# Kernel optimization log

Measured on AMD Instinct MI355X. Metric: run time of the kernel, lower is better.

Reference implementation:

```python
import jax, jax.numpy as jnp
import numpy as np

IN_CH, OUT_CH, SUPPORT = 128, 128, 3
BS, N = 8, 2048


def knn_idx(x, k):
    # x: (bs, n, d) -> (bs, n, k) indices of k nearest (excluding self)
    sq = jnp.sum(x * x, axis=-1)  # (bs, n)
    dist = sq[:, :, None] + sq[:, None, :] - 2.0 * jnp.einsum('bnd,bmd->bnm', x, x)
    _, idx = jax.lax.top_k(-dist, k + 1)  # smallest distances
    return idx[:, :, 1:]


def gather_neighbors(t, idx):
    # t: (bs, n, d), idx: (bs, n, k) -> (bs, n, k, d)
    return jax.vmap(lambda tb, ib: tb[ib])(t, idx)


def l2_normalize(x, axis, eps=1e-12):
    n = jnp.linalg.norm(x, axis=axis, keepdims=True)
    return x / jnp.maximum(n, eps)


def setup_inputs() -> dict:
    key = jax.random.key(0)
    ks = jax.random.split(key, 8)
    stdv = 1.0 / np.sqrt(OUT_CH * (SUPPORT + 1))
    return {
        'vertices': jax.random.normal(ks[0], (BS, N, 3), jnp.float32),
        'feature_map': jax.random.normal(ks[1], (BS, N, IN_CH), jnp.float32),
        'weights': jax.random.uniform(ks[2], (IN_CH, (SUPPORT + 1) * OUT_CH), jnp.float32, -stdv, stdv),
        'bias': jax.random.uniform(ks[3], ((SUPPORT + 1) * OUT_CH,), jnp.float32, -stdv, stdv),
        'directions': jax.random.uniform(ks[4], (3, SUPPORT * OUT_CH), jnp.float32, -stdv, stdv),
        'ste_w': jax.random.normal(ks[5], (OUT_CH, IN_CH), jnp.float32) * (1.0 / np.sqrt(IN_CH)),
        'conv2_w': jax.random.normal(ks[6], (OUT_CH, 2 * OUT_CH), jnp.float32) * (1.0 / np.sqrt(2 * OUT_CH)),
        'neighbor_num': 16,
    }


def reference(vertices, feature_map, weights, bias, directions, ste_w, conv2_w, neighbor_num):
    bs, n, _ = vertices.shape
    k = neighbor_num

    # STE branch: 1x1 conv == per-point linear
    f_ste = jnp.einsum('bnc,oc->bno', feature_map, ste_w)

    # Receptive fields: KNN in feature space ('RF-F'), directions from vertices
    neighbor_index = knn_idx(feature_map, k)                      # (bs, n, k)
    neighbors = gather_neighbors(vertices, neighbor_index)        # (bs, n, k, 3)
    rf_norm = l2_normalize(neighbors - vertices[:, :, None, :], axis=-1)

    # Graph convolution (3D-GCN style)
    sdn = l2_normalize(directions, axis=0)                        # (3, s*out)
    theta = jax.nn.relu(jnp.einsum('bnkd,dm->bnkm', rf_norm, sdn))  # (bs,n,k,s*out)
    fm = feature_map @ weights + bias                             # (bs,n,(s+1)*out)
    feature_center = fm[:, :, :OUT_CH]
    feature_support = gather_neighbors(fm[:, :, OUT_CH:], neighbor_index)  # (bs,n,k,s*out)
    act = (theta * feature_support).reshape(bs, n, k, SUPPORT, OUT_CH)
    act = jnp.max(act, axis=2)          # max over neighbors
    act = jnp.mean(act, axis=2)         # mean over supports
    feature = feature_center + act      # (bs, n, out)

    # ORL: global context via point-space KNN max-pool
    nb_idx2 = knn_idx(vertices, k)
    pooled = jnp.max(gather_neighbors(feature, nb_idx2), axis=2)  # (bs,n,out)
    f_global = jnp.broadcast_to(jnp.mean(pooled, axis=1, keepdims=True), (bs, n, OUT_CH))
    feat_cat = jnp.concatenate([feature, f_global], axis=-1)      # (bs,n,2*out)
    feature_fuse = jnp.einsum('bnc,oc->bno', feat_cat, conv2_w) + feature

    return feature_fuse + f_ste
```

## Files before the change

### kernel.cpp

```cpp
#include <hip/hip_runtime.h>
#include <hip/hip_bf16.h>

#define BS 8
#define NP 2048
#define CIN 128
#define OC 128
#define NSUP 3
#define KNN 16
#define NC 512
#define SC 384
#define CAND 24

typedef __attribute__((ext_vector_type(8))) short bf16x8;
typedef __attribute__((ext_vector_type(4))) float f32x4;

__device__ inline unsigned short f2bf(float x) {
    __hip_bfloat16 h = __float2bfloat16(x);
    return *reinterpret_cast<unsigned short*>(&h);
}
__device__ inline float bf2f(short s) {
    unsigned u = ((unsigned)(unsigned short)s) << 16;
    return __uint_as_float(u);
}
__device__ inline unsigned fkey(float d, int gi) {
    unsigned u = __float_as_uint(d);
    u ^= (unsigned)((int)u >> 31) | 0x80000000u;
    return (u & 0xFFFFF800u) | (unsigned)gi;
}
__device__ inline unsigned umn(unsigned a, unsigned b) { return a < b ? a : b; }
__device__ inline unsigned umx(unsigned a, unsigned b) { return a > b ? a : b; }
__device__ inline void cswap(unsigned& a, unsigned& b) {
    unsigned t = umn(a, b); b = umx(a, b); a = t;
}
__device__ inline unsigned dpp_prev(unsigned v) {
    return (unsigned)__builtin_amdgcn_update_dpp(0, (int)v, 0x111, 0xF, 0xF, true);
}
__device__ inline unsigned third_smallest8(const unsigned kv[8]) {
    unsigned s0=kv[0],s1=kv[1],s2=kv[2],s3=kv[3],s4=kv[4],s5=kv[5],s6=kv[6],s7=kv[7];
    cswap(s0,s1); cswap(s2,s3); cswap(s4,s5); cswap(s6,s7);
    cswap(s0,s2); cswap(s1,s3); cswap(s4,s6); cswap(s5,s7);
    cswap(s1,s2); cswap(s5,s6); cswap(s0,s4); cswap(s3,s7);
    cswap(s1,s5); cswap(s2,s6);
    cswap(s1,s4); cswap(s3,s6);
    cswap(s2,s4); cswap(s3,s5);
    cswap(s3,s4);
    return s2;
}

__global__ __launch_bounds__(256) void prep_kernel(const float* __restrict__ in,
                                                   float* __restrict__ sq,
                                                   short* __restrict__ outp,
                                                   const float* __restrict__ W,
                                                   const float* __restrict__ conv2,
                                                   const float* __restrict__ stew,
                                                   const float* __restrict__ dirs,
                                                   short* __restrict__ Wt,
                                                   short* __restrict__ conv2b,
                                                   short* __restrict__ stewb,
                                                   float4* __restrict__ sdnn4) {
    const int tid = threadIdx.x;
    if (blockIdx.x < 1024) {
        const int row = blockIdx.x * 16 + (tid >> 4);
        const int seg = tid & 15;
        const float* p = in + (size_t)row * CIN + seg * 8;
        float4 f0 = *(const float4*)p;
        float4 f1 = *(const float4*)(p + 4);
        bf16x8 s;
        s[0] = (short)f2bf(f0.x); s[1] = (short)f2bf(f0.y);
        s[2] = (short)f2bf(f0.z); s[3] = (short)f2bf(f0.w);
        s[4] = (short)f2bf(f1.x); s[5] = (short)f2bf(f1.y);
        s[6] = (short)f2bf(f1.z); s[7] = (short)f2bf(f1.w);
        *(bf16x8*)&outp[(size_t)row * CIN + seg * 8] = s;
        float ss = f0.x*f0.x + f0.y*f0.y + f0.z*f0.z + f0.w*f0.w
                 + f1.x*f1.x + f1.y*f1.y + f1.z*f1.z + f1.w*f1.w;
#pragma unroll
        for (int msk = 1; msk <= 8; msk <<= 1) ss += __shfl_xor(ss, msk);
        if (seg == 0) sq[row] = ss;
    } else if (blockIdx.x < 1472) {
        int idx = (blockIdx.x - 1024) * 256 + tid;
        if (idx < NC * CIN) {
            int n = idx >> 7, k = idx & 127;
            Wt[idx] = (short)f2bf(W[(size_t)k * NC + n]);
        } else if (idx < NC * CIN + OC * 2 * OC) {
            int e = idx - NC * CIN;
            conv2b[e] = (short)f2bf(conv2[e]);
        } else {
            int e = idx - NC * CIN - OC * 2 * OC;
            stewb[e] = (short)f2bf(stew[e]);
        }
    } else {
        int m = (blockIdx.x - 1472) * 256 + tid;
        if (m < SC) {
            float d0 = dirs[m], d1 = dirs[SC + m], d2 = dirs[2 * SC + m];
            float nrm = sqrtf(d0 * d0 + d1 * d1 + d2 * d2);
            float den = fmaxf(nrm, 1e-12f);
            sdnn4[m] = make_float4(d0 / den, d1 / den, d2 / den, 0.f);
        }
    }
}

#define TQF 32
#define TPF 64
#define NCHF (NP / TPF)
#define SMEM_BYTES 33536
__global__ __launch_bounds__(256) void fused_kernel(const short* __restrict__ fbb,
                                                    const float* __restrict__ sqn,
                                                    int* __restrict__ cand,
                                                    const float* __restrict__ vert,
                                                    int* __restrict__ nbr2,
                                                    const short* __restrict__ Wt,
                                                    const float* __restrict__ bias,
                                                    float* __restrict__ centerf,
                                                    short* __restrict__ supb) {
    __shared__ alignas(16) unsigned char smem[SMEM_BYTES];
    const int bx = blockIdx.x;
    const int tid = threadIdx.x;
    const int lane = tid & 63, wid = tid >> 6;

    if (bx < 512) {
        short (*Qb)[128]   = (short (*)[128])smem;
        short (*Pb)[128]   = (short (*)[128])(smem + 8192);
        float* sqP         = (float*)(smem + 24576);
        unsigned (*Ds)[68] = (unsigned (*)[68])(smem + 24832);

        const int b = bx >> 6, q0 = (bx & 63) * TQF;
        const short* fb = fbb + (size_t)b * NP * CIN;

        unsigned l0 = 0xFFFFFFFFu, l1 = 0xFFFFFFFFu, l2 = 0xFFFFFFFFu;
        unsigned T = 0xFFFFFFFFu;
        const int gbase = lane & 56;
        const int sub = lane & 7;

        for (int i = 0; i < 2; ++i) {
            int v = i * 256 + tid, row = v >> 4, g = v & 15;
            *(bf16x8*)&Qb[row][(g ^ (row & 7)) * 8] =
                *(const bf16x8*)&fb[(size_t)(q0 + row) * CIN + g * 8];
        }
        for (int i = 0; i < 4; ++i) {
            int v = i * 256 + tid, row = v >> 4, g = v & 15;
            *(bf16x8*)&Pb[row][(g ^ (row & 7)) * 8] =
                *(const bf16x8*)&fb[(size_t)row * CIN + g * 8];
        }
        if (tid < TPF) sqP[tid] = sqn[b * NP + tid];

        const int qt = wid >> 1, ph = wid & 1;
        const int qsl = tid >> 3;
        const int arow = qt * 16 + (lane & 15), asw = arow & 7;
        const int brow0 = ph * 32 + (lane & 15), brow1 = brow0 + 16;
        const int bsw0 = brow0 & 7, bsw1 = brow1 & 7;
        const int oct = lane >> 4;
        const int qrow = qt * 16 + oct * 4;

        for (int ch = 0; ch < NCHF; ++ch) {
            __syncthreads();
            bf16x8 st0, st1, st2, st3;
            float sq_next = 0.f;
            const int nxt = (ch + 1 < NCHF);
            if (nxt) {
                int p0n = (ch + 1) * TPF;
                { int v = tid;       int row = v>>4, g = v&15; st0 = *(const bf16x8*)&fb[(size_t)(p0n+row)*CIN + g*8]; }
                { int v = 256 + tid; int row = v>>4, g = v&15; st1 = *(const bf16x8*)&fb[(size_t)(p0n+row)*CIN + g*8]; }
                { int v = 512 + tid; int row = v>>4, g = v&15; st2 = *(const bf16x8*)&fb[(size_t)(p0n+row)*CIN + g*8]; }
                { int v = 768 + tid; int row = v>>4, g = v&15; st3 = *(const bf16x8*)&fb[(size_t)(p0n+row)*CIN + g*8]; }
                if (tid < TPF) sq_next = sqn[b * NP + p0n + tid];
            }
            f32x4 acc0 = {0.f,0.f,0.f,0.f}, acc1 = {0.f,0.f,0.f,0.f};
#pragma unroll
            for (int kk = 0; kk < 4; ++kk) {
                int g = kk * 4 + oct;
                bf16x8 av  = *(const bf16x8*)&Qb[arow][(g ^ asw) * 8];
                bf16x8 bv0 = *(const bf16x8*)&Pb[brow0][(g ^ bsw0) * 8];
                bf16x8 bv1 = *(const bf16x8*)&Pb[brow1][(g ^ bsw1) * 8];
                acc0 = __builtin_amdgcn_mfma_f32_16x16x32_bf16(av, bv0, acc0, 0, 0, 0);
                acc1 = __builtin_amdgcn_mfma_f32_16x16x32_bf16(av, bv1, acc1, 0, 0, 0);
            }
            const float sp0 = sqP[brow0], sp1 = sqP[brow1];
            const int pg0 = ch * TPF + brow0, pg1 = ch * TPF + brow1;
#pragma unroll
            for (int r = 0; r < 4; ++r) {
                int qg = q0 + qrow + r;
                unsigned k0 = fkey(sp0 - 2.0f * acc0[r], pg0);
                unsigned k1 = fkey(sp1 - 2.0f * acc1[r], pg1);
                if (qg == pg0) k0 = 0xFFFFFFFFu;
                if (qg == pg1) k1 = 0xFFFFFFFFu;
                Ds[qrow + r][brow0] = k0;
                Ds[qrow + r][brow1] = k1;
            }
            __syncthreads();
            {
                uint4 kA = *(const uint4*)&Ds[qsl][sub * 8];
                uint4 kB = *(const uint4*)&Ds[qsl][sub * 8 + 4];
                unsigned kv[8] = {kA.x, kA.y, kA.z, kA.w, kB.x, kB.y, kB.z, kB.w};
                if (ch == 0) {
                    unsigned m3 = third_smallest8(kv);
                    m3 = umx(m3, (unsigned)__shfl_xor((int)m3, 1));
                    m3 = umx(m3, (unsigned)__shfl_xor((int)m3, 2));
                    m3 = umx(m3, (unsigned)__shfl_xor((int)m3, 4));
                    T = m3 + 1;
                }
#pragma unroll
                for (int j = 0; j < 8; ++j) {
                    unsigned long long bal = __ballot(kv[j] < T);
                    unsigned gm = (unsigned)(bal >> gbase) & 0xFFu;
                    while (gm) {
                        int l = __builtin_ctz(gm);
                        gm &= gm - 1;
                        unsigned k = (unsigned)__shfl((int)kv[j], gbase + l);
                        unsigned pv = dpp_prev(l2);
                        if (sub == 0) pv = 0u;
                        unsigned n0 = umn(umx(pv, k), l0);
                        unsigned n1 = umn(umx(l0, k), l1);
                        unsigned n2 = umn(umx(l1, k), l2);
                        l0 = n0; l1 = n1; l2 = n2;
                    }
                }
                T = (unsigned)__shfl((int)l2, gbase + 7);
            }
            if (nxt) {
                { int v = tid;       int row = v>>4, g = v&15; *(bf16x8*)&Pb[row][(g^(row&7))*8] = st0; }
                { int v = 256 + tid; int row = v>>4, g = v&15; *(bf16x8*)&Pb[row][(g^(row&7))*8] = st1; }
                { int v = 512 + tid; int row = v>>4, g = v&15; *(bf16x8*)&Pb[row][(g^(row&7))*8] = st2; }
                { int v = 768 + tid; int row = v>>4, g = v&15; *(bf16x8*)&Pb[row][(g^(row&7))*8] = st3; }
                if (tid < TPF) sqP[tid] = sq_next;
            }
        }
        {
            int* dst = cand + ((size_t)b * NP + q0 + qsl) * CAND;
            dst[3 * sub + 0] = (int)(l0 & 0x7FFu);
            dst[3 * sub + 1] = (int)(l1 & 0x7FFu);
            dst[3 * sub + 2] = (int)(l2 & 0x7FFu);
        }
    } else if (bx < 1024) {
        float* vx = (float*)smem;
        float* vy = (float*)(smem + 8192);
        float* vz = (float*)(smem + 16384);
        const int bb = bx - 512;
        const int b = bb >> 6, q0 = (bb & 63) * 32;
        const float* vb = vert + (size_t)b * NP * 3;

        for (int i = 0; i < NP * 3 / 256; ++i) {
            int e = i * 256 + tid;
            float v = vb[e];
            int row = e / 3, comp = e % 3;
            (comp == 0 ? vx : comp == 1 ? vy : vz)[row] = v;
        }
        __syncthreads();

        const int gbase = lane & 56;
        const int q = tid >> 3;
        const int sub = tid & 7;
        const float qx = vx[q0 + q], qy = vy[q0 + q], qz = vz[q0 + q];

        unsigned l0 = 0xFFFFFFFFu, l1 = 0xFFFFFFFFu, l2 = 0xFFFFFFFFu;
        unsigned T = 0xFFFFFFFFu;

        for (int m = 0; m < NP / 64; ++m) {
            const int p0 = m * 64 + sub * 8;
            float4 xA = *(const float4*)&vx[p0], xB = *(const float4*)&vx[p0 + 4];
            float4 yA = *(const float4*)&vy[p0], yB = *(const float4*)&vy[p0 + 4];
            float4 zA = *(const float4*)&vz[p0], zB = *(const float4*)&vz[p0 + 4];
            float dv[8];
            { float dx = qx-xA.x, dy = qy-yA.x, dz = qz-zA.x; dv[0] = dx*dx+dy*dy+dz*dz; }
            { float dx = qx-xA.y, dy = qy-yA.y, dz = qz-zA.y; dv[1] = dx*dx+dy*dy+dz*dz; }
            { float dx = qx-xA.z, dy = qy-yA.z, dz = qz-zA.z; dv[2] = dx*dx+dy*dy+dz*dz; }
            { float dx = qx-xA.w, dy = qy-yA.w, dz = qz-zA.w; dv[3] = dx*dx+dy*dy+dz*dz; }
            { float dx = qx-xB.x, dy = qy-yB.x, dz = qz-zB.x; dv[4] = dx*dx+dy*dy+dz*dz; }
            { float dx = qx-xB.y, dy = qy-yB.y, dz = qz-zB.y; dv[5] = dx*dx+dy*dy+dz*dz; }
            { float dx = qx-xB.z, dy = qy-yB.z, dz = qz-zB.z; dv[6] = dx*dx+dy*dy+dz*dz; }
            { float dx = qx-xB.w, dy = qy-yB.w, dz = qz-zB.w; dv[7] = dx*dx+dy*dy+dz*dz; }
            unsigned kv[8];
#pragma unroll
            for (int j = 0; j < 8; ++j) kv[j] = fkey(dv[j], p0 + j);
            if (m == 0) {
                unsigned m3 = third_smallest8(kv);
                m3 = umx(m3, (unsigned)__shfl_xor((int)m3, 1));
                m3 = umx(m3, (unsigned)__shfl_xor((int)m3, 2));
                m3 = umx(m3, (unsigned)__shfl_xor((int)m3, 4));
                T = m3 + 1;
            }
#pragma unroll
            for (int j = 0; j < 8; ++j) {
                unsigned long long bal = __ballot(kv[j] < T);
                unsigned gm = (unsigned)(bal >> gbase) & 0xFFu;
                while (gm) {
                    int l = __builtin_ctz(gm);
                    gm &= gm - 1;
                    unsigned k = (unsigned)__shfl((int)kv[j], gbase + l);
                    unsigned pv = dpp_prev(l2);
                    if (sub == 0) pv = 0u;
                    unsigned n0 = umn(umx(pv, k), l0);
                    unsigned n1 = umn(umx(l0, k), l1);
                    unsigned n2 = umn(umx(l1, k), l2);
                    l0 = n0; l1 = n1; l2 = n2;
                }
            }
            T = (unsigned)__shfl((int)l2, gbase + 7);
        }
        {
            int* dst = nbr2 + ((size_t)b * NP + q0 + q) * KNN;
            unsigned vals[3] = {l0, l1, l2};
#pragma unroll
            for (int e = 0; e < 3; ++e) {
                int r = 3 * sub + e;
                if (r >= 1 && r <= 16) dst[r - 1] = (int)(vals[e] & 0x7FFu);
            }
        }
    } else {
        short (*As)[128] = (short (*)[128])smem;
        const int bb = bx - 1024;
        const int m0 = (bb & 255) * 64, n0 = (bb >> 8) * 128;
        const int oct = lane >> 4;
        for (int i = 0; i < 4; ++i) {
            int v = i * 256 + tid, row = v >> 4, g = v & 15;
            *(bf16x8*)&As[row][(g ^ (row & 7)) * 8] =
                *(const bf16x8*)&fbb[(size_t)(m0 + row) * CIN + g * 8];
        }
        __syncthreads();
        f32x4 acc[4][2] = {};
#pragma unroll
        for (int kk = 0; kk < 4; ++kk) {
            int g = kk * 4 + oct;
            bf16x8 bv[2];
#pragma unroll
            for (int nt = 0; nt < 2; ++nt) {
                int n = n0 + (wid * 2 + nt) * 16 + (lane & 15);
                bv[nt] = *(const bf16x8*)&Wt[(size_t)n * CIN + g * 8];
            }
#pragma unroll
            for (int mt = 0; mt < 4; ++mt) {
                int ar = mt * 16 + (lane & 15);
                bf16x8 av = *(const bf16x8*)&As[ar][(g ^ (ar & 7)) * 8];
#pragma unroll
                for (int nt = 0; nt < 2; ++nt)
                    acc[mt][nt] = __builtin_amdgcn_mfma_f32_16x16x32_bf16(av, bv[nt], acc[mt][nt], 0, 0, 0);
            }
        }
#pragma unroll
        for (int mt = 0; mt < 4; ++mt)
#pragma unroll
            for (int nt = 0; nt < 2; ++nt) {
                int n = n0 + (wid * 2 + nt) * 16 + (lane & 15);
                float bsv = bias[n];
                int mbase = m0 + mt * 16 + oct * 4;
#pragma unroll
                for (int r = 0; r < 4; ++r) {
                    float val = acc[mt][nt][r] + bsv;
                    if (n0 == 0)
                        centerf[(size_t)(mbase + r) * OC + n] = val;
                    else
                        supb[(size_t)(mbase + r) * SC + (n - OC)] = (short)f2bf(val);
                }
            }
    }
}

__global__ __launch_bounds__(256) void knn_refine_kernel(const float* __restrict__ feat,
                                                         const int* __restrict__ cand,
                                                         int* __restrict__ nbr) {
    __shared__ unsigned long long keyS[4][CAND];
    const int w = threadIdx.x >> 6;
    const int lane = threadIdx.x & 63;
    const int grp = lane >> 4, sl = lane & 15;
    const int gq = blockIdx.x * 4 + w;
    const int b = gq >> 11;
    const int q = gq & (NP - 1);
    const float* fb = feat + (size_t)b * NP * CIN;

    double qd[8];
    {
        float4 a = *(const float4*)&fb[(size_t)q * CIN + sl * 8];
        float4 c = *(const float4*)&fb[(size_t)q * CIN + sl * 8 + 4];
        qd[0] = a.x; qd[1] = a.y; qd[2] = a.z; qd[3] = a.w;
        qd[4] = c.x; qd[5] = c.y; qd[6] = c.z; qd[7] = c.w;
    }
    double sqd = 0.0;
#pragma unroll
    for (int i = 0; i < 8; ++i) sqd += qd[i] * qd[i];
#pragma unroll
    for (int msk = 1; msk <= 8; msk <<= 1) sqd += __shfl_xor(sqd, msk);
    const float sqi = (float)sqd;

    const int* cq = cand + (size_t)gq * CAND;
    int jv[CAND / 4];
#pragma unroll
    for (int t = 0; t < CAND / 4; ++t) jv[t] = cq[t * 4 + grp];

#pragma unroll
    for (int t = 0; t < CAND / 4; ++t) {
        const int j = jv[t];
        float4 a = *(const float4*)&fb[(size_t)j * CIN + sl * 8];
        float4 c = *(const float4*)&fb[(size_t)j * CIN + sl * 8 + 4];
        double fd[8] = {a.x, a.y, a.z, a.w, c.x, c.y, c.z, c.w};
        double dot = 0.0, sj = 0.0;
#pragma unroll
        for (int i = 0; i < 8; ++i) { dot += qd[i] * fd[i]; sj += fd[i] * fd[i]; }
#pragma unroll
        for (int msk = 1; msk <= 8; msk <<= 1) {
            dot += __shfl_xor(dot, msk);
            sj  += __shfl_xor(sj, msk);
        }
        if (sl == 0) {
            float t1 = sqi + (float)sj;
            float t2 = (float)(2.0 * dot);
            float d32 = t1 - t2;
            unsigned u = __float_as_uint(d32);
            u ^= (unsigned)((int)u >> 31) | 0x80000000u;
            keyS[w][t * 4 + grp] = ((unsigned long long)u << 32) | (unsigned)j;
        }
    }
    __syncthreads();
    if (lane < CAND) {
        unsigned long long k = keyS[w][lane];
        int rank = 0;
#pragma unroll
        for (int m = 0; m < CAND; ++m) rank += (keyS[w][m] < k) ? 1 : 0;
        if (rank < KNN) nbr[(size_t)gq * KNN + rank] = (int)(k & 0xFFFFFFFFu);
    }
}

__global__ __launch_bounds__(128) void act_kernel(const float* __restrict__ centerf,
                                                  const short* __restrict__ supb,
                                                  const int* __restrict__ nbr,
                                                  const float* __restrict__ vert,
                                                  const float4* __restrict__ sdnn4,
                                                  float* __restrict__ feature,
                                                  short* __restrict__ featb) {
    __shared__ int sj[KNN];
    __shared__ float rf[KNN][4];
    const int i = blockIdx.x;
    const int b = blockIdx.y;
    const int tid = threadIdx.x;
    const size_t bi = (size_t)b * NP + i;
    if (tid < KNN) {
        int j = nbr[bi * KNN + tid];
        sj[tid] = j;
        const float* vb = vert + (size_t)b * NP * 3;
        float dx = vb[j * 3 + 0] - vb[i * 3 + 0];
        float dy = vb[j * 3 + 1] - vb[i * 3 + 1];
        float dz = vb[j * 3 + 2] - vb[i * 3 + 2];
        float nrm = sqrtf(dx * dx + dy * dy + dz * dz);
        float den = fmaxf(nrm, 1e-12f);
        rf[tid][0] = dx / den; rf[tid][1] = dy / den; rf[tid][2] = dz / den;
    }
    __syncthreads();
    const int oc = tid;
    float accm = 0.0f;
#pragma unroll
    for (int s = 0; s < NSUP; ++s) {
        int m = s * OC + oc;
        float4 sv = sdnn4[m];
        float s0 = sv.x, s1 = sv.y, s2 = sv.z;
        float vm[4] = {-3.0e38f, -3.0e38f, -3.0e38f, -3.0e38f};
#pragma unroll
        for (int kk = 0; kk < KNN; ++kk) {
            float th = fmaxf(rf[kk][0] * s0 + rf[kk][1] * s1 + rf[kk][2] * s2, 0.0f);
            float sup = bf2f(supb[((size_t)b * NP + sj[kk]) * SC + m]);
            vm[kk & 3] = fmaxf(vm[kk & 3], th * sup);
        }
        accm += fmaxf(fmaxf(vm[0], vm[1]), fmaxf(vm[2], vm[3]));
    }
    float v = centerf[bi * OC + oc] + accm / 3.0f;
    feature[bi * OC + oc] = v;
    featb[bi * OC + oc] = (short)f2bf(v);
}

__global__ __launch_bounds__(128) void pool_kernel(const short* __restrict__ featb,
                                                   const int* __restrict__ nbr2,
                                                   float* __restrict__ pooled) {
    __shared__ int sj[KNN];
    const int i = blockIdx.x, b = blockIdx.y, tid = threadIdx.x;
    const size_t bi = (size_t)b * NP + i;
    if (tid < KNN) sj[tid] = nbr2[bi * KNN + tid];
    __syncthreads();
    float m0 = -3.0e38f, m1 = -3.0e38f, m2 = -3.0e38f, m3 = -3.0e38f;
#pragma unroll
    for (int kk = 0; kk < KNN; kk += 4) {
        m0 = fmaxf(m0, bf2f(featb[((size_t)b * NP + sj[kk + 0]) * OC + tid]));
        m1 = fmaxf(m1, bf2f(featb[((size_t)b * NP + sj[kk + 1]) * OC + tid]));
        m2 = fmaxf(m2, bf2f(featb[((size_t)b * NP + sj[kk + 2]) * OC + tid]));
        m3 = fmaxf(m3, bf2f(featb[((size_t)b * NP + sj[kk + 3]) * OC + tid]));
    }
    pooled[bi * OC + tid] = fmaxf(fmaxf(m0, m1), fmaxf(m2, m3));
}

__global__ __launch_bounds__(128) void partial_kernel(const float* __restrict__ pooled,
                                                      float* __restrict__ part) {
    const int ch = blockIdx.x, b = blockIdx.y, tid = threadIdx.x;
    float s0 = 0.f, s1 = 0.f, s2 = 0.f, s3 = 0.f;
    const float* base = pooled + ((size_t)b * NP + ch * 128) * OC + tid;
    for (int i = 0; i < 128; i += 4) {
        s0 += base[(size_t)(i + 0) * OC];
        s1 += base[(size_t)(i + 1) * OC];
        s2 += base[(size_t)(i + 2) * OC];
        s3 += base[(size_t)(i + 3) * OC];
    }
    part[((size_t)b * 16 + ch) * OC + tid] = ((s0 + s1) + (s2 + s3));
}
__global__ __launch_bounds__(128) void fg_gdot_kernel(const float* __restrict__ part,
                                                      const float* __restrict__ conv2,
                                                      float* __restrict__ gd) {
    __shared__ float fgs[OC];
    const int b = blockIdx.x, tid = threadIdx.x;
    float s = 0.f;
#pragma unroll
    for (int c = 0; c < 16; ++c) s += part[((size_t)b * 16 + c) * OC + tid];
    fgs[tid] = s / (float)NP;
    __syncthreads();
    float g = 0.f;
    const float* w = conv2 + (size_t)tid * 2 * OC + OC;
    for (int c = 0; c < OC; ++c) g += fgs[c] * w[c];
    gd[b * OC + tid] = g;
}

__global__ __launch_bounds__(256) void final_kernel(const short* __restrict__ featb,
                                                    const short* __restrict__ fbb,
                                                    const short* __restrict__ conv2b,
                                                    const short* __restrict__ stewb,
                                                    const float* __restrict__ gd,
                                                    const float* __restrict__ feature,
                                                    float* __restrict__ out) {
    __shared__ alignas(16) short Af[32][128];
    __shared__ alignas(16) short Am[32][128];
    const int m0 = blockIdx.x * 32, tid = threadIdx.x;
    const int lane = tid & 63, wid = tid >> 6, oct = lane >> 4;
    for (int i = 0; i < 2; ++i) {
        int v = i * 256 + tid, row = v >> 4, g = v & 15;
        *(bf16x8*)&Af[row][(g ^ (row & 7)) * 8] =
            *(const bf16x8*)&featb[(size_t)(m0 + row) * OC + g * 8];
        *(bf16x8*)&Am[row][(g ^ (row & 7)) * 8] =
            *(const bf16x8*)&fbb[(size_t)(m0 + row) * CIN + g * 8];
    }
    __syncthreads();
    f32x4 acc[2][2] = {};
#pragma unroll
    for (int kk = 0; kk < 4; ++kk) {
        int g = kk * 4 + oct;
        bf16x8 bC[2], bS[2];
#pragma unroll
        for (int nt = 0; nt < 2; ++nt) {
            int n = (wid * 2 + nt) * 16 + (lane & 15);
            bC[nt] = *(const bf16x8*)&conv2b[(size_t)n * (2 * OC) + g * 8];
            bS[nt] = *(const bf16x8*)&stewb[(size_t)n * CIN + g * 8];
        }
#pragma unroll
        for (int mt = 0; mt < 2; ++mt) {
            int ar = mt * 16 + (lane & 15);
            bf16x8 aF = *(const bf16x8*)&Af[ar][(g ^ (ar & 7)) * 8];
            bf16x8 aM = *(const bf16x8*)&Am[ar][(g ^ (ar & 7)) * 8];
#pragma unroll
            for (int nt = 0; nt < 2; ++nt) {
                acc[mt][nt] = __builtin_amdgcn_mfma_f32_16x16x32_bf16(aF, bC[nt], acc[mt][nt], 0, 0, 0);
                acc[mt][nt] = __builtin_amdgcn_mfma_f32_16x16x32_bf16(aM, bS[nt], acc[mt][nt], 0, 0, 0);
            }
        }
    }
#pragma unroll
    for (int mt = 0; mt < 2; ++mt)
#pragma unroll
        for (int nt = 0; nt < 2; ++nt) {
            int o = (wid * 2 + nt) * 16 + (lane & 15);
            int mbase = m0 + mt * 16 + oct * 4;
#pragma unroll
            for (int r = 0; r < 4; ++r) {
                int m = mbase + r;
                out[(size_t)m * OC + o] = acc[mt][nt][r]
                    + gd[(m >> 11) * OC + o] + feature[(size_t)m * OC + o];
            }
        }
}

extern "C" void kernel_launch(void* const* d_in, const int* in_sizes, int n_in,
                              void* d_out, int out_size, void* d_ws, size_t ws_size,
                              hipStream_t stream) {
    const float* vert  = (const float*)d_in[0];
    const float* fmap  = (const float*)d_in[1];
    const float* W     = (const float*)d_in[2];
    const float* bias  = (const float*)d_in[3];
    const float* dirs  = (const float*)d_in[4];
    const float* stew  = (const float*)d_in[5];
    const float* conv2 = (const float*)d_in[6];
    float* out = (float*)d_out;

    float* ws      = (float*)d_ws;
    float* sqn     = ws;
    short* fbb     = (short*)(sqn + 16384);
    float* centerf = sqn + 16384 + 1048576;
    short* supb    = (short*)(centerf + 2097152);
    float* feature = centerf + 2097152 + 3145728;
    short* featb   = (short*)(feature + 2097152);
    float* gd      = feature + 2097152 + 1048576;
    short* Wt      = (short*)(gd + 1024);
    short* conv2b  = Wt + 65536;
    short* stewb   = conv2b + 32768;
    int*   nbr1    = (int*)(stewb + 16384);
    int*   nbr2    = nbr1 + 262144;
    float* part    = (float*)(nbr2 + 262144);
    float4* sdnn4  = (float4*)(part + 16384);
    int*   cand    = (int*)(sdnn4 + 384);
    float* pooled  = (float*)(cand + 393216);

    prep_kernel<<<1474, 256, 0, stream>>>(fmap, sqn, fbb, W, conv2, stew, dirs,
                                          Wt, conv2b, stewb, sdnn4);
    fused_kernel<<<2048, 256, 0, stream>>>(fbb, sqn, cand, vert, nbr2,
                                           Wt, bias, centerf, supb);
    knn_refine_kernel<<<4096, 256, 0, stream>>>(fmap, cand, nbr1);
    act_kernel<<<dim3(2048, 8), 128, 0, stream>>>(centerf, supb, nbr1, vert, sdnn4,
                                                  feature, featb);
    pool_kernel<<<dim3(2048, 8), 128, 0, stream>>>(featb, nbr2, pooled);
    partial_kernel<<<dim3(16, 8), 128, 0, stream>>>(pooled, part);
    fg_gdot_kernel<<<8, 128, 0, stream>>>(part, conv2, gd);
    final_kernel<<<512, 256, 0, stream>>>(featb, fbb, conv2b, stewb, gd, feature, out);
}
```

Before: 205.9 us.

## Split feature KNN into its own kernel and fuse refinement with vertex KNN and GEMM

The feature-space KNN candidate search moves out of the multi-role fused kernel into a dedicated 512-block kernel. The fp64 candidate refinement is merged into a second multi-role kernel alongside the vertex KNN and the weight GEMM. The aim is to let the long-running feature KNN blocks run alone, then overlap the refinement with the independent vertex KNN and GEMM work, while keeping the same number of launches. In exchange, the vertex KNN and GEMM no longer overlap with the feature KNN search, and the new kernel's shared-memory footprint changes its occupancy.

```diff
diff --git a/kernel.cpp b/kernel.cpp
--- a/kernel.cpp
+++ b/kernel.cpp
@@ -102,139 +102,204 @@
 #define TQF 32
 #define TPF 64
 #define NCHF (NP / TPF)
-#define SMEM_BYTES 33536
-__global__ __launch_bounds__(256) void fused_kernel(const short* __restrict__ fbb,
-                                                    const float* __restrict__ sqn,
-                                                    int* __restrict__ cand,
-                                                    const float* __restrict__ vert,
-                                                    int* __restrict__ nbr2,
-                                                    const short* __restrict__ Wt,
-                                                    const float* __restrict__ bias,
-                                                    float* __restrict__ centerf,
-                                                    short* __restrict__ supb) {
-    __shared__ alignas(16) unsigned char smem[SMEM_BYTES];
+__global__ __launch_bounds__(256) void knn_feat_kernel(const short* __restrict__ fbb,
+                                                       const float* __restrict__ sqn,
+                                                       int* __restrict__ cand) {
+    __shared__ alignas(16) short Qb[TQF][128];
+    __shared__ alignas(16) short Pb[TPF][128];
+    __shared__ float sqP[TPF];
+    __shared__ unsigned Ds[TQF][68];
+
+    const int b = blockIdx.y, q0 = blockIdx.x * TQF, tid = threadIdx.x;
+    const int lane = tid & 63, wid = tid >> 6;
+    const short* fb = fbb + (size_t)b * NP * CIN;
+
+    unsigned l0 = 0xFFFFFFFFu, l1 = 0xFFFFFFFFu, l2 = 0xFFFFFFFFu;
+    unsigned T = 0xFFFFFFFFu;
+    const int gbase = lane & 56;
+    const int sub = lane & 7;
+
+    for (int i = 0; i < 2; ++i) {
+        int v = i * 256 + tid, row = v >> 4, g = v & 15;
+        *(bf16x8*)&Qb[row][(g ^ (row & 7)) * 8] =
+            *(const bf16x8*)&fb[(size_t)(q0 + row) * CIN + g * 8];
+    }
+    for (int i = 0; i < 4; ++i) {
+        int v = i * 256 + tid, row = v >> 4, g = v & 15;
+        *(bf16x8*)&Pb[row][(g ^ (row & 7)) * 8] =
+            *(const bf16x8*)&fb[(size_t)row * CIN + g * 8];
+    }
+    if (tid < TPF) sqP[tid] = sqn[b * NP + tid];
+
+    const int qt = wid >> 1, ph = wid & 1;
+    const int qsl = tid >> 3;
+    const int arow = qt * 16 + (lane & 15), asw = arow & 7;
+    const int brow0 = ph * 32 + (lane & 15), brow1 = brow0 + 16;
+    const int bsw0 = brow0 & 7, bsw1 = brow1 & 7;
+    const int oct = lane >> 4;
+    const int qrow = qt * 16 + oct * 4;
+
+    for (int ch = 0; ch < NCHF; ++ch) {
+        __syncthreads();
+        bf16x8 st0, st1, st2, st3;
+        float sq_next = 0.f;
+        const int nxt = (ch + 1 < NCHF);
+        if (nxt) {
+            int p0n = (ch + 1) * TPF;
+            { int v = tid;       int row = v>>4, g = v&15; st0 = *(const bf16x8*)&fb[(size_t)(p0n+row)*CIN + g*8]; }
+            { int v = 256 + tid; int row = v>>4, g = v&15; st1 = *(const bf16x8*)&fb[(size_t)(p0n+row)*CIN + g*8]; }
+            { int v = 512 + tid; int row = v>>4, g = v&15; st2 = *(const bf16x8*)&fb[(size_t)(p0n+row)*CIN + g*8]; }
+            { int v = 768 + tid; int row = v>>4, g = v&15; st3 = *(const bf16x8*)&fb[(size_t)(p0n+row)*CIN + g*8]; }
+            if (tid < TPF) sq_next = sqn[b * NP + p0n + tid];
+        }
+        f32x4 acc0 = {0.f,0.f,0.f,0.f}, acc1 = {0.f,0.f,0.f,0.f};
+#pragma unroll
+        for (int kk = 0; kk < 4; ++kk) {
+            int g = kk * 4 + oct;
+            bf16x8 av  = *(const bf16x8*)&Qb[arow][(g ^ asw) * 8];
+            bf16x8 bv0 = *(const bf16x8*)&Pb[brow0][(g ^ bsw0) * 8];
+            bf16x8 bv1 = *(const bf16x8*)&Pb[brow1][(g ^ bsw1) * 8];
+            acc0 = __builtin_amdgcn_mfma_f32_16x16x32_bf16(av, bv0, acc0, 0, 0, 0);
+            acc1 = __builtin_amdgcn_mfma_f32_16x16x32_bf16(av, bv1, acc1, 0, 0, 0);
+        }
+        const float sp0 = sqP[brow0], sp1 = sqP[brow1];
+        const int pg0 = ch * TPF + brow0, pg1 = ch * TPF + brow1;
+#pragma unroll
+        for (int r = 0; r < 4; ++r) {
+            int qg = q0 + qrow + r;
+            unsigned k0 = fkey(sp0 - 2.0f * acc0[r], pg0);
+            unsigned k1 = fkey(sp1 - 2.0f * acc1[r], pg1);
+            if (qg == pg0) k0 = 0xFFFFFFFFu;
+            if (qg == pg1) k1 = 0xFFFFFFFFu;
+            Ds[qrow + r][brow0] = k0;
+            Ds[qrow + r][brow1] = k1;
+        }
+        __syncthreads();
+        {
+            uint4 kA = *(const uint4*)&Ds[qsl][sub * 8];
+            uint4 kB = *(const uint4*)&Ds[qsl][sub * 8 + 4];
+            unsigned kv[8] = {kA.x, kA.y, kA.z, kA.w, kB.x, kB.y, kB.z, kB.w};
+            if (ch == 0) {
+                unsigned m3 = third_smallest8(kv);
+                m3 = umx(m3, (unsigned)__shfl_xor((int)m3, 1));
+                m3 = umx(m3, (unsigned)__shfl_xor((int)m3, 2));
+                m3 = umx(m3, (unsigned)__shfl_xor((int)m3, 4));
+                T = m3 + 1;
+            }
+#pragma unroll
+            for (int j = 0; j < 8; ++j) {
+                unsigned long long bal = __ballot(kv[j] < T);
+                unsigned gm = (unsigned)(bal >> gbase) & 0xFFu;
+                while (gm) {
+                    int l = __builtin_ctz(gm);
+                    gm &= gm - 1;
+                    unsigned k = (unsigned)__shfl((int)kv[j], gbase + l);
+                    unsigned pv = dpp_prev(l2);
+                    if (sub == 0) pv = 0u;
+                    unsigned n0 = umn(umx(pv, k), l0);
+                    unsigned n1 = umn(umx(l0, k), l1);
+                    unsigned n2 = umn(umx(l1, k), l2);
+                    l0 = n0; l1 = n1; l2 = n2;
+                }
+            }
+            T = (unsigned)__shfl((int)l2, gbase + 7);
+        }
+        if (nxt) {
+            { int v = tid;       int row = v>>4, g = v&15; *(bf16x8*)&Pb[row][(g^(row&7))*8] = st0; }
+            { int v = 256 + tid; int row = v>>4, g = v&15; *(bf16x8*)&Pb[row][(g^(row&7))*8] = st1; }
+            { int v = 512 + tid; int row = v>>4, g = v&15; *(bf16x8*)&Pb[row][(g^(row&7))*8] = st2; }
+            { int v = 768 + tid; int row = v>>4, g = v&15; *(bf16x8*)&Pb[row][(g^(row&7))*8] = st3; }
+            if (tid < TPF) sqP[tid] = sq_next;
+        }
+    }
+    {
+        int* dst = cand + ((size_t)b * NP + q0 + qsl) * CAND;
+        dst[3 * sub + 0] = (int)(l0 & 0x7FFu);
+        dst[3 * sub + 1] = (int)(l1 & 0x7FFu);
+        dst[3 * sub + 2] = (int)(l2 & 0x7FFu);
+    }
+}
+
+#define SMEM2 24576
+__global__ __launch_bounds__(256) void fused2_kernel(const float* __restrict__ feat,
+                                                     const int* __restrict__ cand,
+                                                     int* __restrict__ nbr,
+                                                     const float* __restrict__ vert,
+                                                     int* __restrict__ nbr2,
+                                                     const short* __restrict__ fbb,
+                                                     const short* __restrict__ Wt,
+                                                     const float* __restrict__ bias,
+                                                     float* __restrict__ centerf,
+                                                     short* __restrict__ supb) {
+    __shared__ alignas(16) unsigned char smem[SMEM2];
     const int bx = blockIdx.x;
     const int tid = threadIdx.x;
     const int lane = tid & 63, wid = tid >> 6;
 
-    if (bx < 512) {
-        short (*Qb)[128]   = (short (*)[128])smem;
-        short (*Pb)[128]   = (short (*)[128])(smem + 8192);
-        float* sqP         = (float*)(smem + 24576);
-        unsigned (*Ds)[68] = (unsigned (*)[68])(smem + 24832);
-
-        const int b = bx >> 6, q0 = (bx & 63) * TQF;
-        const short* fb = fbb + (size_t)b * NP * CIN;
-
-        unsigned l0 = 0xFFFFFFFFu, l1 = 0xFFFFFFFFu, l2 = 0xFFFFFFFFu;
-        unsigned T = 0xFFFFFFFFu;
-        const int gbase = lane & 56;
-        const int sub = lane & 7;
-
-        for (int i = 0; i < 2; ++i) {
-            int v = i * 256 + tid, row = v >> 4, g = v & 15;
-            *(bf16x8*)&Qb[row][(g ^ (row & 7)) * 8] =
-                *(const bf16x8*)&fb[(size_t)(q0 + row) * CIN + g * 8];
-        }
-        for (int i = 0; i < 4; ++i) {
-            int v = i * 256 + tid, row = v >> 4, g = v & 15;
-            *(bf16x8*)&Pb[row][(g ^ (row & 7)) * 8] =
-                *(const bf16x8*)&fb[(size_t)row * CIN + g * 8];
-        }
-        if (tid < TPF) sqP[tid] = sqn[b * NP + tid];
-
-        const int qt = wid >> 1, ph = wid & 1;
-        const int qsl = tid >> 3;
-        const int arow = qt * 16 + (lane & 15), asw = arow & 7;
-        const int brow0 = ph * 32 + (lane & 15), brow1 = brow0 + 16;
-        const int bsw0 = brow0 & 7, bsw1 = brow1 & 7;
-        const int oct = lane >> 4;
-        const int qrow = qt * 16 + oct * 4;
-
-        for (int ch = 0; ch < NCHF; ++ch) {
-            __syncthreads();
-            bf16x8 st0, st1, st2, st3;
-            float sq_next = 0.f;
-            const int nxt = (ch + 1 < NCHF);
-            if (nxt) {
-                int p0n = (ch + 1) * TPF;
-                { int v = tid;       int row = v>>4, g = v&15; st0 = *(const bf16x8*)&fb[(size_t)(p0n+row)*CIN + g*8]; }
-                { int v = 256 + tid; int row = v>>4, g = v&15; st1 = *(const bf16x8*)&fb[(size_t)(p0n+row)*CIN + g*8]; }
-                { int v = 512 + tid; int row = v>>4, g = v&15; st2 = *(const bf16x8*)&fb[(size_t)(p0n+row)*CIN + g*8]; }
-                { int v = 768 + tid; int row = v>>4, g = v&15; st3 = *(const bf16x8*)&fb[(size_t)(p0n+row)*CIN + g*8]; }
-                if (tid < TPF) sq_next = sqn[b * NP + p0n + tid];
-            }
-            f32x4 acc0 = {0.f,0.f,0.f,0.f}, acc1 = {0.f,0.f,0.f,0.f};
-#pragma unroll
-            for (int kk = 0; kk < 4; ++kk) {
-                int g = kk * 4 + oct;
-                bf16x8 av  = *(const bf16x8*)&Qb[arow][(g ^ asw) * 8];
-                bf16x8 bv0 = *(const bf16x8*)&Pb[brow0][(g ^ bsw0) * 8];
-                bf16x8 bv1 = *(const bf16x8*)&Pb[brow1][(g ^ bsw1) * 8];
-                acc0 = __builtin_amdgcn_mfma_f32_16x16x32_bf16(av, bv0, acc0, 0, 0, 0);
-                acc1 = __builtin_amdgcn_mfma_f32_16x16x32_bf16(av, bv1, acc1, 0, 0, 0);
-            }
-            const float sp0 = sqP[brow0], sp1 = sqP[brow1];
-            const int pg0 = ch * TPF + brow0, pg1 = ch * TPF + brow1;
-#pragma unroll
-            for (int r = 0; r < 4; ++r) {
-                int qg = q0 + qrow + r;
-                unsigned k0 = fkey(sp0 - 2.0f * acc0[r], pg0);
-                unsigned k1 = fkey(sp1 - 2.0f * acc1[r], pg1);
-                if (qg == pg0) k0 = 0xFFFFFFFFu;
-                if (qg == pg1) k1 = 0xFFFFFFFFu;
-                Ds[qrow + r][brow0] = k0;
-                Ds[qrow + r][brow1] = k1;
-            }
-            __syncthreads();
-            {
-                uint4 kA = *(const uint4*)&Ds[qsl][sub * 8];
-                uint4 kB = *(const uint4*)&Ds[qsl][sub * 8 + 4];
-                unsigned kv[8] = {kA.x, kA.y, kA.z, kA.w, kB.x, kB.y, kB.z, kB.w};
-                if (ch == 0) {
-                    unsigned m3 = third_smallest8(kv);
-                    m3 = umx(m3, (unsigned)__shfl_xor((int)m3, 1));
-                    m3 = umx(m3, (unsigned)__shfl_xor((int)m3, 2));
-                    m3 = umx(m3, (unsigned)__shfl_xor((int)m3, 4));
-                    T = m3 + 1;
-                }
-#pragma unroll
-                for (int j = 0; j < 8; ++j) {
-                    unsigned long long bal = __ballot(kv[j] < T);
-                    unsigned gm = (unsigned)(bal >> gbase) & 0xFFu;
-                    while (gm) {
-                        int l = __builtin_ctz(gm);
-                        gm &= gm - 1;
-                        unsigned k = (unsigned)__shfl((int)kv[j], gbase + l);
-                        unsigned pv = dpp_prev(l2);
-                        if (sub == 0) pv = 0u;
-                        unsigned n0 = umn(umx(pv, k), l0);
-                        unsigned n1 = umn(umx(l0, k), l1);
-                        unsigned n2 = umn(umx(l1, k), l2);
-                        l0 = n0; l1 = n1; l2 = n2;
-                    }
-                }
-                T = (unsigned)__shfl((int)l2, gbase + 7);
-            }
-            if (nxt) {
-                { int v = tid;       int row = v>>4, g = v&15; *(bf16x8*)&Pb[row][(g^(row&7))*8] = st0; }
-                { int v = 256 + tid; int row = v>>4, g = v&15; *(bf16x8*)&Pb[row][(g^(row&7))*8] = st1; }
-                { int v = 512 + tid; int row = v>>4, g = v&15; *(bf16x8*)&Pb[row][(g^(row&7))*8] = st2; }
-                { int v = 768 + tid; int row = v>>4, g = v&15; *(bf16x8*)&Pb[row][(g^(row&7))*8] = st3; }
-                if (tid < TPF) sqP[tid] = sq_next;
-            }
-        }
+    if (bx < 4096) {
+        unsigned long long (*keyS)[CAND] = (unsigned long long (*)[CAND])smem;
+        const int w = wid;
+        const int grp = lane >> 4, sl = lane & 15;
+        const int gq = bx * 4 + w;
+        const int b = gq >> 11;
+        const int q = gq & (NP - 1);
+        const float* fb = feat + (size_t)b * NP * CIN;
+
+        double qd[8];
         {
-            int* dst = cand + ((size_t)b * NP + q0 + qsl) * CAND;
-            dst[3 * sub + 0] = (int)(l0 & 0x7FFu);
-            dst[3 * sub + 1] = (int)(l1 & 0x7FFu);
-            dst[3 * sub + 2] = (int)(l2 & 0x7FFu);
-        }
-    } else if (bx < 1024) {
+            float4 a = *(const float4*)&fb[(size_t)q * CIN + sl * 8];
+            float4 c = *(const float4*)&fb[(size_t)q * CIN + sl * 8 + 4];
+            qd[0] = a.x; qd[1] = a.y; qd[2] = a.z; qd[3] = a.w;
+            qd[4] = c.x; qd[5] = c.y; qd[6] = c.z; qd[7] = c.w;
+        }
+        double sqd = 0.0;
+#pragma unroll
+        for (int i = 0; i < 8; ++i) sqd += qd[i] * qd[i];
+#pragma unroll
+        for (int msk = 1; msk <= 8; msk <<= 1) sqd += __shfl_xor(sqd, msk);
+        const float sqi = (float)sqd;
+
+        const int* cq = cand + (size_t)gq * CAND;
+        int jv[CAND / 4];
+#pragma unroll
+        for (int t = 0; t < CAND / 4; ++t) jv[t] = cq[t * 4 + grp];
+
+#pragma unroll
+        for (int t = 0; t < CAND / 4; ++t) {
+            const int j = jv[t];
+            float4 a = *(const float4*)&fb[(size_t)j * CIN + sl * 8];
+            float4 c = *(const float4*)&fb[(size_t)j * CIN + sl * 8 + 4];
+            double fd[8] = {a.x, a.y, a.z, a.w, c.x, c.y, c.z, c.w};
+            double dot = 0.0, sj = 0.0;
+#pragma unroll
+            for (int i = 0; i < 8; ++i) { dot += qd[i] * fd[i]; sj += fd[i] * fd[i]; }
+#pragma unroll
+            for (int msk = 1; msk <= 8; msk <<= 1) {
+                dot += __shfl_xor(dot, msk);
+                sj  += __shfl_xor(sj, msk);
+            }
+            if (sl == 0) {
+                float t1 = sqi + (float)sj;
+                float t2 = (float)(2.0 * dot);
+                float d32 = t1 - t2;
+                unsigned u = __float_as_uint(d32);
+                u ^= (unsigned)((int)u >> 31) | 0x80000000u;
+                keyS[w][t * 4 + grp] = ((unsigned long long)u << 32) | (unsigned)j;
+            }
+        }
+        __syncthreads();
+        if (lane < CAND) {
+            unsigned long long k = keyS[w][lane];
+            int rank = 0;
+#pragma unroll
+            for (int m = 0; m < CAND; ++m) rank += (keyS[w][m] < k) ? 1 : 0;
+            if (rank < KNN) nbr[(size_t)gq * KNN + rank] = (int)(k & 0xFFFFFFFFu);
+        }
+    } else if (bx < 4608) {
         float* vx = (float*)smem;
         float* vy = (float*)(smem + 8192);
         float* vz = (float*)(smem + 16384);
-        const int bb = bx - 512;
+        const int bb = bx - 4096;
         const int b = bb >> 6, q0 = (bb & 63) * 32;
         const float* vb = vert + (size_t)b * NP * 3;
 
@@ -307,7 +372,7 @@
         }
     } else {
         short (*As)[128] = (short (*)[128])smem;
-        const int bb = bx - 1024;
+        const int bb = bx - 4608;
         const int m0 = (bb & 255) * 64, n0 = (bb >> 8) * 128;
         const int oct = lane >> 4;
         for (int i = 0; i < 4; ++i) {
@@ -351,70 +416,6 @@
                         supb[(size_t)(mbase + r) * SC + (n - OC)] = (short)f2bf(val);
                 }
             }
-    }
-}
-
-__global__ __launch_bounds__(256) void knn_refine_kernel(const float* __restrict__ feat,
-                                                         const int* __restrict__ cand,
-                                                         int* __restrict__ nbr) {
-    __shared__ unsigned long long keyS[4][CAND];
-    const int w = threadIdx.x >> 6;
-    const int lane = threadIdx.x & 63;
-    const int grp = lane >> 4, sl = lane & 15;
-    const int gq = blockIdx.x * 4 + w;
-    const int b = gq >> 11;
-    const int q = gq & (NP - 1);
-    const float* fb = feat + (size_t)b * NP * CIN;
-
-    double qd[8];
-    {
-        float4 a = *(const float4*)&fb[(size_t)q * CIN + sl * 8];
-        float4 c = *(const float4*)&fb[(size_t)q * CIN + sl * 8 + 4];
-        qd[0] = a.x; qd[1] = a.y; qd[2] = a.z; qd[3] = a.w;
-        qd[4] = c.x; qd[5] = c.y; qd[6] = c.z; qd[7] = c.w;
-    }
-    double sqd = 0.0;
-#pragma unroll
-    for (int i = 0; i < 8; ++i) sqd += qd[i] * qd[i];
-#pragma unroll
-    for (int msk = 1; msk <= 8; msk <<= 1) sqd += __shfl_xor(sqd, msk);
-    const float sqi = (float)sqd;
-
-    const int* cq = cand + (size_t)gq * CAND;
-    int jv[CAND / 4];
-#pragma unroll
-    for (int t = 0; t < CAND / 4; ++t) jv[t] = cq[t * 4 + grp];
-
-#pragma unroll
-    for (int t = 0; t < CAND / 4; ++t) {
-        const int j = jv[t];
-        float4 a = *(const float4*)&fb[(size_t)j * CIN + sl * 8];
-        float4 c = *(const float4*)&fb[(size_t)j * CIN + sl * 8 + 4];
-        double fd[8] = {a.x, a.y, a.z, a.w, c.x, c.y, c.z, c.w};
-        double dot = 0.0, sj = 0.0;
-#pragma unroll
-        for (int i = 0; i < 8; ++i) { dot += qd[i] * fd[i]; sj += fd[i] * fd[i]; }
-#pragma unroll
-        for (int msk = 1; msk <= 8; msk <<= 1) {
-            dot += __shfl_xor(dot, msk);
-            sj  += __shfl_xor(sj, msk);
-        }
-        if (sl == 0) {
-            float t1 = sqi + (float)sj;
-            float t2 = (float)(2.0 * dot);
-            float d32 = t1 - t2;
-            unsigned u = __float_as_uint(d32);
-            u ^= (unsigned)((int)u >> 31) | 0x80000000u;
-            keyS[w][t * 4 + grp] = ((unsigned long long)u << 32) | (unsigned)j;
-        }
-    }
-    __syncthreads();
-    if (lane < CAND) {
-        unsigned long long k = keyS[w][lane];
-        int rank = 0;
-#pragma unroll
-        for (int m = 0; m < CAND; ++m) rank += (keyS[w][m] < k) ? 1 : 0;
-        if (rank < KNN) nbr[(size_t)gq * KNN + rank] = (int)(k & 0xFFFFFFFFu);
     }
 }
 
@@ -601,9 +602,9 @@
 
     prep_kernel<<<1474, 256, 0, stream>>>(fmap, sqn, fbb, W, conv2, stew, dirs,
                                           Wt, conv2b, stewb, sdnn4);
-    fused_kernel<<<2048, 256, 0, stream>>>(fbb, sqn, cand, vert, nbr2,
-                                           Wt, bias, centerf, supb);
-    knn_refine_kernel<<<4096, 256, 0, stream>>>(fmap, cand, nbr1);
+    knn_feat_kernel<<<dim3(64, 8), 256, 0, stream>>>(fbb, sqn, cand);
+    fused2_kernel<<<5632, 256, 0, stream>>>(fmap, cand, nbr1, vert, nbr2,
+                                            fbb, Wt, bias, centerf, supb);
     act_kernel<<<dim3(2048, 8), 128, 0, stream>>>(centerf, supb, nbr1, vert, sdnn4,
                                                   feature, featb);
     pool_kernel<<<dim3(2048, 8), 128, 0, stream>>>(featb, nbr2, pooled);
```

Result: slower. 210.6 us (+2.3%).

## Regroup fused kernels: move point-space KNN alongside feature-KNN refine

Applied to the files above, without the earlier changes.

The point-space KNN blocks move out of the first fused kernel, which now holds only the feature-space candidate search and the weight GEMM. They go into a new second kernel that also runs the candidate refinement. The refine step switches from 16 lanes per candidate with 8 elements each to 8 lanes with 16 elements, which shortens the shuffle reductions. The aim is to balance the work across the two launches and fill the second launch's tail with independent vertex KNN work. The price is more registers per lane in the refine path and different LDS sizing per kernel.

```diff
diff --git a/kernel.cpp b/kernel.cpp
--- a/kernel.cpp
+++ b/kernel.cpp
@@ -102,17 +102,15 @@
 #define TQF 32
 #define TPF 64
 #define NCHF (NP / TPF)
-#define SMEM_BYTES 33536
-__global__ __launch_bounds__(256) void fused_kernel(const short* __restrict__ fbb,
-                                                    const float* __restrict__ sqn,
-                                                    int* __restrict__ cand,
-                                                    const float* __restrict__ vert,
-                                                    int* __restrict__ nbr2,
-                                                    const short* __restrict__ Wt,
-                                                    const float* __restrict__ bias,
-                                                    float* __restrict__ centerf,
-                                                    short* __restrict__ supb) {
-    __shared__ alignas(16) unsigned char smem[SMEM_BYTES];
+#define SMEMA 33536
+__global__ __launch_bounds__(256) void fusedA_kernel(const short* __restrict__ fbb,
+                                                     const float* __restrict__ sqn,
+                                                     int* __restrict__ cand,
+                                                     const short* __restrict__ Wt,
+                                                     const float* __restrict__ bias,
+                                                     float* __restrict__ centerf,
+                                                     short* __restrict__ supb) {
+    __shared__ alignas(16) unsigned char smem[SMEMA];
     const int bx = blockIdx.x;
     const int tid = threadIdx.x;
     const int lane = tid & 63, wid = tid >> 6;
@@ -230,11 +228,140 @@
             dst[3 * sub + 1] = (int)(l1 & 0x7FFu);
             dst[3 * sub + 2] = (int)(l2 & 0x7FFu);
         }
-    } else if (bx < 1024) {
+    } else {
+        short (*As)[128] = (short (*)[128])smem;
+        const int bb = bx - 512;
+        const int m0 = (bb & 255) * 64, n0 = (bb >> 8) * 128;
+        const int oct = lane >> 4;
+        for (int i = 0; i < 4; ++i) {
+            int v = i * 256 + tid, row = v >> 4, g = v & 15;
+            *(bf16x8*)&As[row][(g ^ (row & 7)) * 8] =
+                *(const bf16x8*)&fbb[(size_t)(m0 + row) * CIN + g * 8];
+        }
+        __syncthreads();
+        f32x4 acc[4][2] = {};
+#pragma unroll
+        for (int kk = 0; kk < 4; ++kk) {
+            int g = kk * 4 + oct;
+            bf16x8 bv[2];
+#pragma unroll
+            for (int nt = 0; nt < 2; ++nt) {
+                int n = n0 + (wid * 2 + nt) * 16 + (lane & 15);
+                bv[nt] = *(const bf16x8*)&Wt[(size_t)n * CIN + g * 8];
+            }
+#pragma unroll
+            for (int mt = 0; mt < 4; ++mt) {
+                int ar = mt * 16 + (lane & 15);
+                bf16x8 av = *(const bf16x8*)&As[ar][(g ^ (ar & 7)) * 8];
+#pragma unroll
+                for (int nt = 0; nt < 2; ++nt)
+                    acc[mt][nt] = __builtin_amdgcn_mfma_f32_16x16x32_bf16(av, bv[nt], acc[mt][nt], 0, 0, 0);
+            }
+        }
+#pragma unroll
+        for (int mt = 0; mt < 4; ++mt)
+#pragma unroll
+            for (int nt = 0; nt < 2; ++nt) {
+                int n = n0 + (wid * 2 + nt) * 16 + (lane & 15);
+                float bsv = bias[n];
+                int mbase = m0 + mt * 16 + oct * 4;
+#pragma unroll
+                for (int r = 0; r < 4; ++r) {
+                    float val = acc[mt][nt][r] + bsv;
+                    if (n0 == 0)
+                        centerf[(size_t)(mbase + r) * OC + n] = val;
+                    else
+                        supb[(size_t)(mbase + r) * SC + (n - OC)] = (short)f2bf(val);
+                }
+            }
+    }
+}
+
+#define SMEMB 24576
+__global__ __launch_bounds__(256) void fusedB_kernel(const float* __restrict__ feat,
+                                                     const int* __restrict__ cand,
+                                                     int* __restrict__ nbr,
+                                                     const float* __restrict__ vert,
+                                                     int* __restrict__ nbr2) {
+    __shared__ alignas(16) unsigned char smem[SMEMB];
+    const int bx = blockIdx.x;
+    const int tid = threadIdx.x;
+    const int lane = tid & 63, wid = tid >> 6;
+
+    if (bx < 4096) {
+        unsigned long long (*keyS)[CAND] = (unsigned long long (*)[CAND])smem;
+        const int w = wid;
+        const int gc = lane >> 3, sl = lane & 7;
+        const int gq = bx * 4 + w;
+        const int b = gq >> 11;
+        const int q = gq & (NP - 1);
+        const float* fb = feat + (size_t)b * NP * CIN;
+
+        float qf[16];
+        *(float4*)&qf[0]  = *(const float4*)&fb[(size_t)q * CIN + sl * 16 + 0];
+        *(float4*)&qf[4]  = *(const float4*)&fb[(size_t)q * CIN + sl * 16 + 4];
+        *(float4*)&qf[8]  = *(const float4*)&fb[(size_t)q * CIN + sl * 16 + 8];
+        *(float4*)&qf[12] = *(const float4*)&fb[(size_t)q * CIN + sl * 16 + 12];
+        double sa = 0.0, sb = 0.0;
+#pragma unroll
+        for (int i = 0; i < 8; ++i) {
+            sa += (double)qf[i] * (double)qf[i];
+            sb += (double)qf[8 + i] * (double)qf[8 + i];
+        }
+        double sqd = sa + sb;
+#pragma unroll
+        for (int msk = 1; msk <= 4; msk <<= 1) sqd += __shfl_xor(sqd, msk);
+        const float sqi = (float)sqd;
+
+        const int* cq = cand + (size_t)gq * CAND;
+        int jv[3];
+#pragma unroll
+        for (int t = 0; t < 3; ++t) jv[t] = cq[t * 8 + gc];
+
+#pragma unroll
+        for (int t = 0; t < 3; ++t) {
+            const int j = jv[t];
+            float cf[16];
+            *(float4*)&cf[0]  = *(const float4*)&fb[(size_t)j * CIN + sl * 16 + 0];
+            *(float4*)&cf[4]  = *(const float4*)&fb[(size_t)j * CIN + sl * 16 + 4];
+            *(float4*)&cf[8]  = *(const float4*)&fb[(size_t)j * CIN + sl * 16 + 8];
+            *(float4*)&cf[12] = *(const float4*)&fb[(size_t)j * CIN + sl * 16 + 12];
+            double d0 = 0.0, d1 = 0.0, e0 = 0.0, e1 = 0.0;
+#pragma unroll
+            for (int i = 0; i < 8; ++i) {
+                d0 += (double)qf[i] * (double)cf[i];
+                e0 += (double)cf[i] * (double)cf[i];
+                d1 += (double)qf[8 + i] * (double)cf[8 + i];
+                e1 += (double)cf[8 + i] * (double)cf[8 + i];
+            }
+            double dot = d0 + d1, sj = e0 + e1;
+#pragma unroll
+            for (int msk = 1; msk <= 4; msk <<= 1) {
+                dot += __shfl_xor(dot, msk);
+                sj  += __shfl_xor(sj, msk);
+            }
+            if (sl == 0) {
+                float t1 = sqi + (float)sj;
+                float t2 = (float)(2.0 * dot);
+                float d32 = t1 - t2;
+                unsigned u = __float_as_uint(d32);
+                u ^= (unsigned)((int)u >> 31) | 0x80000000u;
+                keyS[w][t * 8 + gc] = ((unsigned long long)u << 32) | (unsigned)j;
+            }
+        }
+        __syncthreads();
+        if (lane < CAND) {
+            unsigned long long k = keyS[w][lane];
+            int rank = 0;
+#pragma unroll
+            for (int m = 0; m < CAND; ++m) rank += (keyS[w][m] < k) ? 1 : 0;
+            if (rank < KNN) nbr[(size_t)gq * KNN + rank] = (int)(k & 0xFFFFFFFFu);
+        }
+    } else {
         float* vx = (float*)smem;
         float* vy = (float*)(smem + 8192);
         float* vz = (float*)(smem + 16384);
-        const int bb = bx - 512;
+        const int bb = bx - 4096;
         const int b = bb >> 6, q0 = (bb & 63) * 32;
         const float* vb = vert + (size_t)b * NP * 3;
 
@@ -305,116 +432,6 @@
                 if (r >= 1 && r <= 16) dst[r - 1] = (int)(vals[e] & 0x7FFu);
             }
         }
-    } else {
-        short (*As)[128] = (short (*)[128])smem;
-        const int bb = bx - 1024;
-        const int m0 = (bb & 255) * 64, n0 = (bb >> 8) * 128;
-        const int oct = lane >> 4;
-        for (int i = 0; i < 4; ++i) {
-            int v = i * 256 + tid, row = v >> 4, g = v & 15;
-            *(bf16x8*)&As[row][(g ^ (row & 7)) * 8] =
-                *(const bf16x8*)&fbb[(size_t)(m0 + row) * CIN + g * 8];
-        }
-        __syncthreads();
-        f32x4 acc[4][2] = {};
-#pragma unroll
-        for (int kk = 0; kk < 4; ++kk) {
-            int g = kk * 4 + oct;
-            bf16x8 bv[2];
-#pragma unroll
-            for (int nt = 0; nt < 2; ++nt) {
-                int n = n0 + (wid * 2 + nt) * 16 + (lane & 15);
-                bv[nt] = *(const bf16x8*)&Wt[(size_t)n * CIN + g * 8];
-            }
-#pragma unroll
-            for (int mt = 0; mt < 4; ++mt) {
-                int ar = mt * 16 + (lane & 15);
-                bf16x8 av = *(const bf16x8*)&As[ar][(g ^ (ar & 7)) * 8];
-#pragma unroll
-                for (int nt = 0; nt < 2; ++nt)
-                    acc[mt][nt] = __builtin_amdgcn_mfma_f32_16x16x32_bf16(av, bv[nt], acc[mt][nt], 0, 0, 0);
-            }
-        }
-#pragma unroll
-        for (int mt = 0; mt < 4; ++mt)
-#pragma unroll
-            for (int nt = 0; nt < 2; ++nt) {
-                int n = n0 + (wid * 2 + nt) * 16 + (lane & 15);
-                float bsv = bias[n];
-                int mbase = m0 + mt * 16 + oct * 4;
-#pragma unroll
-                for (int r = 0; r < 4; ++r) {
-                    float val = acc[mt][nt][r] + bsv;
-                    if (n0 == 0)
-                        centerf[(size_t)(mbase + r) * OC + n] = val;
-                    else
-                        supb[(size_t)(mbase + r) * SC + (n - OC)] = (short)f2bf(val);
-                }
-            }
-    }
-}
-
-__global__ __launch_bounds__(256) void knn_refine_kernel(const float* __restrict__ feat,
-                                                         const int* __restrict__ cand,
-                                                         int* __restrict__ nbr) {
-    __shared__ unsigned long long keyS[4][CAND];
-    const int w = threadIdx.x >> 6;
-    const int lane = threadIdx.x & 63;
-    const int grp = lane >> 4, sl = lane & 15;
-    const int gq = blockIdx.x * 4 + w;
-    const int b = gq >> 11;
-    const int q = gq & (NP - 1);
-    const float* fb = feat + (size_t)b * NP * CIN;
-
-    double qd[8];
-    {
-        float4 a = *(const float4*)&fb[(size_t)q * CIN + sl * 8];
-        float4 c = *(const float4*)&fb[(size_t)q * CIN + sl * 8 + 4];
-        qd[0] = a.x; qd[1] = a.y; qd[2] = a.z; qd[3] = a.w;
-        qd[4] = c.x; qd[5] = c.y; qd[6] = c.z; qd[7] = c.w;
-    }
-    double sqd = 0.0;
-#pragma unroll
-    for (int i = 0; i < 8; ++i) sqd += qd[i] * qd[i];
-#pragma unroll
-    for (int msk = 1; msk <= 8; msk <<= 1) sqd += __shfl_xor(sqd, msk);
-    const float sqi = (float)sqd;
-
-    const int* cq = cand + (size_t)gq * CAND;
-    int jv[CAND / 4];
-#pragma unroll
-    for (int t = 0; t < CAND / 4; ++t) jv[t] = cq[t * 4 + grp];
-
-#pragma unroll
-    for (int t = 0; t < CAND / 4; ++t) {
-        const int j = jv[t];
-        float4 a = *(const float4*)&fb[(size_t)j * CIN + sl * 8];
-        float4 c = *(const float4*)&fb[(size_t)j * CIN + sl * 8 + 4];
-        double fd[8] = {a.x, a.y, a.z, a.w, c.x, c.y, c.z, c.w};
-        double dot = 0.0, sj = 0.0;
-#pragma unroll
-        for (int i = 0; i < 8; ++i) { dot += qd[i] * fd[i]; sj += fd[i] * fd[i]; }
-#pragma unroll
-        for (int msk = 1; msk <= 8; msk <<= 1) {
-            dot += __shfl_xor(dot, msk);
-            sj  += __shfl_xor(sj, msk);
-        }
-        if (sl == 0) {
-            float t1 = sqi + (float)sj;
-            float t2 = (float)(2.0 * dot);
-            float d32 = t1 - t2;
-            unsigned u = __float_as_uint(d32);
-            u ^= (unsigned)((int)u >> 31) | 0x80000000u;
-            keyS[w][t * 4 + grp] = ((unsigned long long)u << 32) | (unsigned)j;
-        }
-    }
-    __syncthreads();
-    if (lane < CAND) {
-        unsigned long long k = keyS[w][lane];
-        int rank = 0;
-#pragma unroll
-        for (int m = 0; m < CAND; ++m) rank += (keyS[w][m] < k) ? 1 : 0;
-        if (rank < KNN) nbr[(size_t)gq * KNN + rank] = (int)(k & 0xFFFFFFFFu);
     }
 }
 
@@ -601,9 +618,8 @@
 
     prep_kernel<<<1474, 256, 0, stream>>>(fmap, sqn, fbb, W, conv2, stew, dirs,
                                           Wt, conv2b, stewb, sdnn4);
-    fused_kernel<<<2048, 256, 0, stream>>>(fbb, sqn, cand, vert, nbr2,
-                                           Wt, bias, centerf, supb);
-    knn_refine_kernel<<<4096, 256, 0, stream>>>(fmap, cand, nbr1);
+    fusedA_kernel<<<1536, 256, 0, stream>>>(fbb, sqn, cand, Wt, bias, centerf, supb);
+    fusedB_kernel<<<4608, 256, 0, stream>>>(fmap, cand, nbr1, vert, nbr2);
     act_kernel<<<dim3(2048, 8), 128, 0, stream>>>(centerf, supb, nbr1, vert, sdnn4,
                                                   feature, featb);
     pool_kernel<<<dim3(2048, 8), 128, 0, stream>>>(featb, nbr2, pooled);
```

Result: slower. 213.1 us (+3.5%).
